# Optimization experiments

Hardware: AMD Instinct MI355X
Metric: run time of the kernel (lower is better)

The kernel has to match this reference:

```python
import jax, jax.numpy as jnp
import numpy as np

NL = 8  # number of wavenet cells


def _causal_dil_conv(x, w, b, dil):
    # x: (B, Cin, T), w: (Cout, Cin, K) -> (B, Cout, T), left-padded (causal)
    pad = (w.shape[-1] - 1) * dil
    y = jax.lax.conv_general_dilated(
        x, w, window_strides=(1,), padding=[(pad, 0)],
        rhs_dilation=(dil,), dimension_numbers=('NCH', 'OIH', 'NCH'))
    return y + b[None, :, None]


def setup_inputs() -> dict:
    key = jax.random.key(0)
    ks = jax.random.split(key, 12)
    T, B, d_lag, d_cov, d, K = 2048, 16, 1, 7, 256, 2
    s = 0.05
    return {
        'x_lag': jax.random.normal(ks[0], (T, B, d_lag), jnp.float32),
        'x_cov': jax.random.normal(ks[1], (T, B, d_cov), jnp.float32),
        'up_W': jax.random.normal(ks[2], (d_lag + d_cov, d), jnp.float32) * s,
        'up_b': jax.random.normal(ks[3], (d,), jnp.float32) * s,
        'dil_w': jax.random.normal(ks[4], (NL, 2 * d, d, K), jnp.float32) * s,
        'dil_b': jax.random.normal(ks[5], (NL, 2 * d), jnp.float32) * s,
        'skip_w': jax.random.normal(ks[6], (NL, 2 * d, d, 1), jnp.float32) * s,
        'skip_b': jax.random.normal(ks[7], (NL, 2 * d), jnp.float32) * s,
        'loc_W': jax.random.normal(ks[8], (d, 1), jnp.float32) * s,
        'loc_b': jax.random.normal(ks[9], (1,), jnp.float32) * s,
        'proj_W': jax.random.normal(ks[10], (1, 1), jnp.float32) * s,
        'proj_b': jax.random.normal(ks[11], (1,), jnp.float32) * s,
        'd_outputseqlen': 96,
    }


def reference(x_lag, x_cov, up_W, up_b, dil_w, dil_b, skip_w, skip_b,
              loc_W, loc_b, proj_W, proj_b, d_outputseqlen):
    T = x_lag.shape[0]
    h = jnp.concatenate([x_lag, x_cov[:T]], axis=-1)          # (T,B,d_lag+d_cov)
    h = h @ up_W + up_b                                        # (T,B,d)
    h = jnp.transpose(h, (1, 2, 0))                            # (B,d,T)
    skip = jnp.zeros_like(h)
    for i in range(NL):
        z = _causal_dil_conv(h, dil_w[i], dil_b[i], 2 ** i)    # (B,2d,T)
        f, g = jnp.split(z, 2, axis=1)
        gated = jnp.tanh(f) * jax.nn.sigmoid(g)                # (B,d,T)
        z2 = _causal_dil_conv(gated, skip_w[i], skip_b[i], 1)  # (B,2d,T)
        h_next, skip_next = jnp.split(z2, 2, axis=1)
        h = h + h_next
        skip = skip + skip_next
    out = jnp.transpose(skip[:, :, -d_outputseqlen:], (2, 0, 1))  # (L,B,d)
    loc = out @ loc_W + loc_b                                     # (L,B,1)
    y = jnp.transpose(loc, (1, 0, 2))[..., None]                  # (B,L,1,1)
    return y @ proj_W + proj_b                                    # (B,L,1,c_out)
```

## Files before the change

kernel.cpp:

```cpp
#include <hip/hip_runtime.h>
#include <math.h>
#include <stdint.h>

#define T_TOTAL 2048
#define NB 16
#define D 256
#define T0 1696
#define TBUF 352
#define TSKIP 1952
#define LOUT 96

typedef __bf16 bf16x8 __attribute__((ext_vector_type(8)));
typedef __bf16 bf16x4v __attribute__((ext_vector_type(4)));
typedef float f32x4 __attribute__((ext_vector_type(4)));

__device__ __forceinline__ void gload_lds16(const void* src, void* lds_dst) {
    auto g = (const __attribute__((address_space(1))) void*)(uintptr_t)src;
    auto l = (__attribute__((address_space(3))) void*)(uintptr_t)(
                 (uint32_t)(uintptr_t)lds_dst);
    __builtin_amdgcn_global_load_lds(g, l, 16, 0, 0);
}

__device__ __forceinline__ void decode_tile(int id, int ngate, int& rt, int& ct) {
    int k = id & 7;
    int j = id >> 3;
    int rpx = ngate >> 6;
    rt = k * rpx + (j >> 3);
    ct = j & 7;
}

__global__ __launch_bounds__(256) void prep_up(
    const float* __restrict__ dil_w, const float* __restrict__ skip_w,
    const float* __restrict__ x_lag, const float* __restrict__ x_cov,
    const float* __restrict__ up_W, const float* __restrict__ up_b,
    const float* __restrict__ loc_W,
    __bf16* __restrict__ wT, __bf16* __restrict__ w2, __bf16* __restrict__ w2T,
    float* __restrict__ hf, __bf16* __restrict__ hb,
    float* __restrict__ vWp)
{
    const int g0 = blockIdx.x * 256 + threadIdx.x;
    const int NT = 2048 * 256;

    for (int u = g0; u < 8 * 512 * 32; u += NT) {
        int j = u & 31;
        int cog = u >> 5;
        const float* src = dil_w + ((size_t)cog << 9) + (j << 4);
        float4 a = *(const float4*)(src);
        float4 b = *(const float4*)(src + 4);
        float4 c = *(const float4*)(src + 8);
        float4 d = *(const float4*)(src + 12);
        bf16x8 t0 = {(__bf16)a.x, (__bf16)a.z, (__bf16)b.x, (__bf16)b.z,
                     (__bf16)c.x, (__bf16)c.z, (__bf16)d.x, (__bf16)d.z};
        bf16x8 t1 = {(__bf16)a.y, (__bf16)a.w, (__bf16)b.y, (__bf16)b.w,
                     (__bf16)c.y, (__bf16)c.w, (__bf16)d.y, (__bf16)d.w};
        *(bf16x8*)(wT + ((size_t)cog << 9) + (j << 3)) = t0;
        *(bf16x8*)(wT + ((size_t)cog << 9) + 256 + (j << 3)) = t1;
    }
    for (int u = g0; u < 5 * 256 * 32; u += NT) {
        int row = u >> 5, j = u & 31;
        int ly = row >> 8, co = row & 255;
        const float* src = skip_w + (((size_t)(ly << 9) + co) << 8) + (j << 3);
        float4 a = *(const float4*)(src);
        float4 b = *(const float4*)(src + 4);
        bf16x8 v = {(__bf16)a.x, (__bf16)a.y, (__bf16)a.z, (__bf16)a.w,
                    (__bf16)b.x, (__bf16)b.y, (__bf16)b.z, (__bf16)b.w};
        *(bf16x8*)(w2 + ((size_t)row << 8) + (j << 3)) = v;
    }
    for (int u = g0; u < 2 * 256 * 32; u += NT) {
        int row = u >> 5, j = u & 31;
        int lyr = row >> 8, co = row & 255;
        int ly = 5 + lyr;
        const float* src = skip_w + (((size_t)(ly << 9) + co) << 8) + (j << 3);
        float4 a = *(const float4*)(src);
        float4 b = *(const float4*)(src + 4);
        float v[8] = {a.x, a.y, a.z, a.w, b.x, b.y, b.z, b.w};
        __bf16* wt = w2T + ((size_t)lyr << 16) + ((size_t)(j << 3) << 8) + co;
        #pragma unroll
        for (int e = 0; e < 8; ++e) wt[(size_t)e << 8] = (__bf16)v[e];
    }
    for (int u = g0; u < TBUF * NB * D; u += NT) {
        int row = u >> 8, c = u & 255;
        int tt = row >> 4, b = row & 15, t = T0 + tt;
        float acc = up_b[c] + x_lag[t * NB + b] * up_W[c];
        const float* cov = &x_cov[(t * NB + b) * 7];
        #pragma unroll
        for (int j = 0; j < 7; ++j)
            acc += cov[j] * up_W[(j + 1) * D + c];
        hf[u] = acc;
        hb[u] = (__bf16)acc;
    }
    for (int u = g0; u < 16384; u += NT) {
        int part = u >> 11;
        int r = u & 2047;
        int ly = r >> 8, ci = r & 255;
        const float* sw = skip_w + (((size_t)(ly << 9) + 256 + (part << 5)) << 8) + ci;
        float acc = 0.f;
        #pragma unroll 8
        for (int c = 0; c < 32; ++c)
            acc += sw[(size_t)c << 8] * loc_W[(part << 5) + c];
        vWp[u] = acc;
    }
}

__global__ __launch_bounds__(512, 4) void d0_kernel(
    const __bf16* __restrict__ hb, __bf16* __restrict__ gated,
    const __bf16* __restrict__ wT, const float* __restrict__ dil_b,
    const __bf16* __restrict__ w2T, const float* __restrict__ skip_b,
    __bf16* __restrict__ V, float* __restrict__ cbias,
    __bf16* __restrict__ gsv, int ngate, int tb, int M)
{
    __shared__ __align__(16) unsigned char lds[32768];
    const int id = blockIdx.x;
    const int tid = threadIdx.x;
    const int lane = tid & 63, wid = tid >> 6;
    const int wm = wid >> 1, wn = wid & 1;
    const int l15 = lane & 15, l4 = lane >> 4;
    const int ach = lane & 7;

    if (id < ngate) {
        int rt, ct;
        decode_tile(id, ngate, rt, ct);
        const int m0 = rt << 6;
        if (m0 >= M) return;
        const int cb = ct << 5;
        const int arow = (wid << 3) + (lane >> 3);
        const int aswz = (ach ^ (arow & 7)) << 3;
        const int bwid = wid & 3, bhalf = wid >> 2;
        const int brow = (bwid << 3) + (lane >> 3);
        const int bswz = (ach ^ (brow & 7)) << 3;
        const int roff1 = (tb - T0) * 16;
        const int roff0 = roff1 - 16;

        f32x4 accf = {}, accg = {};
        auto stage = [&](int t, int buf) {
            const int k0 = t << 6;
            const int ci0 = k0 & 255;
            const int roff = (t < 4) ? roff0 : roff1;
            unsigned char* base = lds + buf * 16384;
            int m = m0 + arow; if (m >= M) m = M - 1;
            gload_lds16(hb + (size_t)(m + roff) * 256 + ci0 + aswz,
                        base + (wid << 10));
            gload_lds16(wT + (size_t)(cb + bhalf * 256 + brow) * 512 + k0 + bswz,
                        base + 8192 + (bhalf << 12) + (bwid << 10));
        };
        stage(0, 0);
        for (int t = 0; t < 8; ++t) {
            const int buf = t & 1;
            if (t < 7) {
                stage(t + 1, buf ^ 1);
                asm volatile("s_waitcnt vmcnt(2)" ::: "memory");
            } else {
                asm volatile("s_waitcnt vmcnt(0)" ::: "memory");
            }
            __builtin_amdgcn_s_barrier();
            const unsigned char* base = lds + buf * 16384;
            __builtin_amdgcn_s_setprio(1);
            #pragma unroll
            for (int ks = 0; ks < 2; ++ks) {
                const int kb = (ks << 6) + (l4 << 4);
                int r = (wm << 4) + l15;
                bf16x8 av = *(const bf16x8*)(base + r * 128 + (kb ^ ((r & 7) << 4)));
                int n = (wn << 4) + l15;
                int o = n * 128 + (kb ^ ((n & 7) << 4));
                bf16x8 bfv = *(const bf16x8*)(base + 8192 + o);
                bf16x8 bgv = *(const bf16x8*)(base + 12288 + o);
                accf = __builtin_amdgcn_mfma_f32_16x16x32_bf16(av, bfv, accf, 0, 0, 0);
                accg = __builtin_amdgcn_mfma_f32_16x16x32_bf16(av, bgv, accg, 0, 0, 0);
            }
            __builtin_amdgcn_s_setprio(0);
            __builtin_amdgcn_s_barrier();
        }
        {
            const int ms0 = (TSKIP - tb) * 16;
            const int soff = (tb - TSKIP) * 16;
            int c = cb + (wn << 4) + l15;
            float bfb = dil_b[c], bgb = dil_b[c + 256];
            #pragma unroll
            for (int r = 0; r < 4; ++r) {
                int m = m0 + (wm << 4) + (l4 << 2) + r;
                if (m < M) {
                    float fv = accf[r] + bfb;
                    float gv = accg[r] + bgb;
                    float th = 2.0f / (1.0f + __expf(-2.0f * fv)) - 1.0f;
                    float sg = 1.0f / (1.0f + __expf(-gv));
                    __bf16 val = (__bf16)(th * sg);
                    gated[(size_t)m * 256 + c] = val;
                    if (m >= ms0)
                        gsv[(size_t)(m + soff) * 256 + c] = val;
                }
            }
        }
    } else if (id < ngate + 384) {
        int v = id - ngate;
        int pair = v >> 7;
        int r = v & 127;
        int tgt = (pair == 0) ? 6 : 7;
        int srcix = (pair == 2) ? 1 : 0;
        int a = r >> 6;
        int rt = (r & 63) >> 3, ct = r & 7;
        const int n0t = rt << 6;
        const int cb = ct << 5;
        const __bf16* Awt = wT + ((size_t)tgt << 18) + (a << 8);
        const __bf16* Bw = w2T + ((size_t)srcix << 16);
        const int arow = (wid << 3) + (lane >> 3);
        const int aswz = (ach ^ (arow & 7)) << 3;
        const int brow = (wid << 3) + (lane >> 3);
        const int bswz = (ach ^ (brow & 7)) << 3;

        f32x4 acc = {};
        auto stage = [&](int t, int buf) {
            const int k0 = t << 6;
            unsigned char* base = lds + buf * 12288;
            gload_lds16(Awt + (size_t)(n0t + arow) * 512 + k0 + aswz,
                        base + (wid << 10));
            if (wid < 4)
                gload_lds16(Bw + (size_t)(cb + brow) * 256 + k0 + bswz,
                            base + 8192 + (wid << 10));
        };
        stage(0, 0);
        for (int t = 0; t < 4; ++t) {
            const int buf = t & 1;
            if (t < 3) {
                stage(t + 1, buf ^ 1);
                if (wid < 4) { asm volatile("s_waitcnt vmcnt(2)" ::: "memory"); }
                else         { asm volatile("s_waitcnt vmcnt(1)" ::: "memory"); }
            } else {
                asm volatile("s_waitcnt vmcnt(0)" ::: "memory");
            }
            __builtin_amdgcn_s_barrier();
            const unsigned char* base = lds + buf * 12288;
            #pragma unroll
            for (int ks = 0; ks < 2; ++ks) {
                const int kb = (ks << 6) + (l4 << 4);
                int rr = (wm << 4) + l15;
                bf16x8 av = *(const bf16x8*)(base + rr * 128 + (kb ^ ((rr & 7) << 4)));
                int nn = (wn << 4) + l15;
                int o = nn * 128 + (kb ^ ((nn & 7) << 4));
                bf16x8 bv = *(const bf16x8*)(base + 8192 + o);
                acc = __builtin_amdgcn_mfma_f32_16x16x32_bf16(av, bv, acc, 0, 0, 0);
            }
            __builtin_amdgcn_s_barrier();
        }
        {
            int c = cb + (wn << 4) + l15;
            #pragma unroll
            for (int rr = 0; rr < 4; ++rr) {
                int n = n0t + (wm << 4) + (l4 << 2) + rr;
                V[((size_t)pair << 18) + (size_t)n * 512 + (a << 8) + c] = (__bf16)acc[rr];
            }
        }
    } else {
        int cblk = id - ngate - 384;
        int n = cblk * 8 + wid;
        int tl = n >> 9, n0 = n & 511;
        const __bf16* wrow = wT + ((size_t)(6 + tl) << 18) + ((size_t)n0 << 9);
        float s = 0.f;
        #pragma unroll
        for (int e = 0; e < 8; ++e) {
            int k = (lane << 3) + e;
            float sbv = skip_b[(5 << 9) + (k & 255)];
            if (tl == 1) sbv += skip_b[(6 << 9) + (k & 255)];
            s += sbv * (float)wrow[k];
        }
        #pragma unroll
        for (int off = 32; off; off >>= 1) s += __shfl_down(s, off);
        if (lane == 0)
            cbias[(tl << 9) + n0] = dil_b[((6 + tl) << 9) + n0] + s;
    }
}

__global__ __launch_bounds__(512, 4) void gate_n32(
    const __bf16* __restrict__ hb, __bf16* __restrict__ gout,
    const __bf16* __restrict__ wTl, const float* __restrict__ gbias,
    __bf16* __restrict__ gsv, int do_save,
    int tb, int dil, int M)
{
    __shared__ __align__(16) unsigned char lds[32768];
    int rt, ct;
    decode_tile(blockIdx.x, gridDim.x, rt, ct);
    const int m0 = rt << 6;
    if (m0 >= M) return;
    const int cb = ct << 5;
    const int tid = threadIdx.x;
    const int lane = tid & 63, wid = tid >> 6;
    const int wm = wid >> 1, wn = wid & 1;
    const int l15 = lane & 15, l4 = lane >> 4;
    const int arow = (wid << 3) + (lane >> 3);
    const int ach = lane & 7;
    const int aswz = (ach ^ (arow & 7)) << 3;
    const int bwid = wid & 3, bhalf = wid >> 2;
    const int brow = (bwid << 3) + (lane >> 3);
    const int bswz = (ach ^ (brow & 7)) << 3;
    const int roff1 = (tb - T0) * 16;
    const int roff0 = roff1 - dil * 16;

    f32x4 accf = {}, accg = {};
    auto stage = [&](int t, int buf) {
        const int k0 = t << 6;
        const int ci0 = k0 & 255;
        const int roff = (t < 4) ? roff0 : roff1;
        unsigned char* base = lds + buf * 16384;
        int m = m0 + arow; if (m >= M) m = M - 1;
        gload_lds16(hb + (size_t)(m + roff) * 256 + ci0 + aswz,
                    base + (wid << 10));
        gload_lds16(wTl + (size_t)(cb + bhalf * 256 + brow) * 512 + k0 + bswz,
                    base + 8192 + (bhalf << 12) + (bwid << 10));
    };
    stage(0, 0);
    for (int t = 0; t < 8; ++t) {
        const int buf = t & 1;
        if (t < 7) {
            stage(t + 1, buf ^ 1);
            asm volatile("s_waitcnt vmcnt(2)" ::: "memory");
        } else {
            asm volatile("s_waitcnt vmcnt(0)" ::: "memory");
        }
        __builtin_amdgcn_s_barrier();
        const unsigned char* base = lds + buf * 16384;
        __builtin_amdgcn_s_setprio(1);
        #pragma unroll
        for (int ks = 0; ks < 2; ++ks) {
            const int kb = (ks << 6) + (l4 << 4);
            int r = (wm << 4) + l15;
            bf16x8 av = *(const bf16x8*)(base + r * 128 + (kb ^ ((r & 7) << 4)));
            int n = (wn << 4) + l15;
            int o = n * 128 + (kb ^ ((n & 7) << 4));
            bf16x8 bfv = *(const bf16x8*)(base + 8192 + o);
            bf16x8 bgv = *(const bf16x8*)(base + 12288 + o);
            accf = __builtin_amdgcn_mfma_f32_16x16x32_bf16(av, bfv, accf, 0, 0, 0);
            accg = __builtin_amdgcn_mfma_f32_16x16x32_bf16(av, bgv, accg, 0, 0, 0);
        }
        __builtin_amdgcn_s_setprio(0);
        __builtin_amdgcn_s_barrier();
    }
    {
        const int ms0 = (TSKIP - tb) * 16;
        const int soff = (tb - TSKIP) * 16;
        int c = cb + (wn << 4) + l15;
        float bfb = gbias[c], bgb = gbias[c + 256];
        #pragma unroll
        for (int r = 0; r < 4; ++r) {
            int m = m0 + (wm << 4) + (l4 << 2) + r;
            if (m < M) {
                float fv = accf[r] + bfb;
                float gv = accg[r] + bgb;
                float th = 2.0f / (1.0f + __expf(-2.0f * fv)) - 1.0f;
                float sg = 1.0f / (1.0f + __expf(-gv));
                __bf16 val = (__bf16)(th * sg);
                gout[(size_t)m * 256 + c] = val;
                if (do_save && m >= ms0)
                    gsv[(size_t)(m + soff) * 256 + c] = val;
            }
        }
    }
}

__global__ __launch_bounds__(512, 4) void gate_sub(
    const __bf16* __restrict__ hb,
    const __bf16* __restrict__ g1, const __bf16* __restrict__ g2,
    __bf16* __restrict__ gout,
    const __bf16* __restrict__ Bh, const __bf16* __restrict__ Bv1,
    const __bf16* __restrict__ Bv2, const float* __restrict__ cbias_l,
    int tb, int dil, int M, int nsteps,
    int hro0, int hro1, int g1o0, int g1o1, int g2o0, int g2o1)
{
    __shared__ __align__(16) unsigned char lds[32768];
    int rt, ct;
    decode_tile(blockIdx.x, gridDim.x, rt, ct);
    const int m0 = rt << 6;
    if (m0 >= M) return;
    const int cb = ct << 5;
    const int tid = threadIdx.x;
    const int lane = tid & 63, wid = tid >> 6;
    const int wm = wid >> 1, wn = wid & 1;
    const int l15 = lane & 15, l4 = lane >> 4;
    const int arow = (wid << 3) + (lane >> 3);
    const int ach = lane & 7;
    const int aswz = (ach ^ (arow & 7)) << 3;
    const int bwid = wid & 3, bhalf = wid >> 2;
    const int brow = (bwid << 3) + (lane >> 3);
    const int bswz = (ach ^ (brow & 7)) << 3;

    f32x4 accf = {}, accg = {};
    auto stage = [&](int t, int buf) {
        unsigned char* base = lds + buf * 16384;
        int m = m0 + arow; if (m >= M) m = M - 1;
        const __bf16* asrc;
        const __bf16* bsrc;
        int ks;
        if (t < 8) {
            ks = t << 6;
            asrc = hb + (size_t)(m + ((t < 4) ? hro0 : hro1)) * 256 + (ks & 255);
            bsrc = Bh;
        } else if (t < 16) {
            ks = (t - 8) << 6;
            asrc = g1 + (size_t)(m + ((t < 12) ? g1o0 : g1o1)) * 256 + (ks & 255);
            bsrc = Bv1;
        } else {
            ks = (t - 16) << 6;
            asrc = g2 + (size_t)(m + ((t < 20) ? g2o0 : g2o1)) * 256 + (ks & 255);
            bsrc = Bv2;
        }
        gload_lds16(asrc + aswz, base + (wid << 10));
        gload_lds16(bsrc + (size_t)(cb + bhalf * 256 + brow) * 512 + ks + bswz,
                    base + 8192 + (bhalf << 12) + (bwid << 10));
    };
    stage(0, 0);
    for (int t = 0; t < nsteps; ++t) {
        const int buf = t & 1;
        if (t < nsteps - 1) {
            stage(t + 1, buf ^ 1);
            asm volatile("s_waitcnt vmcnt(2)" ::: "memory");
        } else {
            asm volatile("s_waitcnt vmcnt(0)" ::: "memory");
        }
        __builtin_amdgcn_s_barrier();
        const unsigned char* base = lds + buf * 16384;
        __builtin_amdgcn_s_setprio(1);
        #pragma unroll
        for (int ks = 0; ks < 2; ++ks) {
            const int kb = (ks << 6) + (l4 << 4);
            int r = (wm << 4) + l15;
            bf16x8 av = *(const bf16x8*)(base + r * 128 + (kb ^ ((r & 7) << 4)));
            int n = (wn << 4) + l15;
            int o = n * 128 + (kb ^ ((n & 7) << 4));
            bf16x8 bfv = *(const bf16x8*)(base + 8192 + o);
            bf16x8 bgv = *(const bf16x8*)(base + 12288 + o);
            accf = __builtin_amdgcn_mfma_f32_16x16x32_bf16(av, bfv, accf, 0, 0, 0);
            accg = __builtin_amdgcn_mfma_f32_16x16x32_bf16(av, bgv, accg, 0, 0, 0);
        }
        __builtin_amdgcn_s_setprio(0);
        __builtin_amdgcn_s_barrier();
    }
    {
        int c = cb + (wn << 4) + l15;
        float bfb = cbias_l[c], bgb = cbias_l[c + 256];
        #pragma unroll
        for (int r = 0; r < 4; ++r) {
            int m = m0 + (wm << 4) + (l4 << 2) + r;
            if (m < M) {
                float fv = accf[r] + bfb;
                float gv = accg[r] + bgb;
                float th = 2.0f / (1.0f + __expf(-2.0f * fv)) - 1.0f;
                float sg = 1.0f / (1.0f + __expf(-gv));
                gout[(size_t)m * 256 + c] = (__bf16)(th * sg);
            }
        }
    }
}

__global__ __launch_bounds__(512, 4) void skip_h(
    const __bf16* __restrict__ gated, const __bf16* __restrict__ w2l,
    float* __restrict__ hf, __bf16* __restrict__ hb,
    const float* __restrict__ sbias, int tb, int M)
{
    __shared__ __align__(16) unsigned char lds[24576];
    int rt, ct;
    decode_tile(blockIdx.x, gridDim.x, rt, ct);
    const int m0 = rt << 6;
    if (m0 >= M) return;
    const int cb = ct << 5;
    const int tid = threadIdx.x;
    const int lane = tid & 63, wid = tid >> 6;
    const int wm = wid >> 1, wn = wid & 1;
    const int l15 = lane & 15, l4 = lane >> 4;
    const int arow = (wid << 3) + (lane >> 3);
    const int ach = lane & 7;
    const int aswz = (ach ^ (arow & 7)) << 3;
    const int brow = (wid << 3) + (lane >> 3);
    const int bswz = (ach ^ (brow & 7)) << 3;
    const int roff1 = (tb - T0) * 16;

    f32x4 acch = {};
    auto stage = [&](int t, int buf) {
        const int k0 = t << 6;
        unsigned char* base = lds + buf * 12288;
        int m = m0 + arow; if (m >= M) m = M - 1;
        gload_lds16(gated + (size_t)m * 256 + k0 + aswz,
                    base + (wid << 10));
        if (wid < 4)
            gload_lds16(w2l + (size_t)(cb + brow) * 256 + k0 + bswz,
                        base + 8192 + (wid << 10));
    };
    stage(0, 0);
    for (int t = 0; t < 4; ++t) {
        const int buf = t & 1;
        if (t < 3) {
            stage(t + 1, buf ^ 1);
            if (wid < 4) { asm volatile("s_waitcnt vmcnt(2)" ::: "memory"); }
            else         { asm volatile("s_waitcnt vmcnt(1)" ::: "memory"); }
        } else {
            asm volatile("s_waitcnt vmcnt(0)" ::: "memory");
        }
        __builtin_amdgcn_s_barrier();
        const unsigned char* base = lds + buf * 12288;
        __builtin_amdgcn_s_setprio(1);
        #pragma unroll
        for (int ks = 0; ks < 2; ++ks) {
            const int kb = (ks << 6) + (l4 << 4);
            int r = (wm << 4) + l15;
            bf16x8 av = *(const bf16x8*)(base + r * 128 + (kb ^ ((r & 7) << 4)));
            int n = (wn << 4) + l15;
            int o = n * 128 + (kb ^ ((n & 7) << 4));
            bf16x8 bhv = *(const bf16x8*)(base + 8192 + o);
            acch = __builtin_amdgcn_mfma_f32_16x16x32_bf16(av, bhv, acch, 0, 0, 0);
        }
        __builtin_amdgcn_s_setprio(0);
        __builtin_amdgcn_s_barrier();
    }
    {
        int c = cb + (wn << 4) + l15;
        float bhb = sbias[c];
        #pragma unroll
        for (int r = 0; r < 4; ++r) {
            int m = m0 + (wm << 4) + (l4 << 2) + r;
            if (m < M) {
                size_t hi = (size_t)(m + roff1) * 256 + c;
                float hv = hf[hi] + acch[r] + bhb;
                hf[hi] = hv;
                hb[hi] = (__bf16)hv;
            }
        }
    }
}

__global__ __launch_bounds__(256) void final_v4(
    const __bf16* __restrict__ gsave, const __bf16* __restrict__ gA,
    const __bf16* __restrict__ gB, const __bf16* __restrict__ g7,
    const float* __restrict__ vWp, const float* __restrict__ skip_b,
    const float* __restrict__ loc_W, const float* __restrict__ loc_b,
    const float* __restrict__ proj_W, const float* __restrict__ proj_b,
    float* __restrict__ out)
{
    int tid = threadIdx.x;
    int wid = tid >> 6, lane = tid & 63;
    int o = blockIdx.x * 4 + wid;
    const __bf16* bases[8] = {
        gsave,                gsave + 1536 * 256,     gsave + 2 * 1536 * 256,
        gsave + 3 * 1536 * 256, gsave + 4 * 1536 * 256,
        gA + 3072 * 256,      gB + 2048 * 256,        g7 };
    float acc = 0.f;
    #pragma unroll
    for (int ly = 0; ly < 8; ++ly) {
        bf16x4v gv = *(const bf16x4v*)(bases[ly] + ((size_t)o << 8) + (lane << 2));
        float4 vw = {0.f, 0.f, 0.f, 0.f};
        #pragma unroll
        for (int p = 0; p < 8; ++p) {
            float4 vp = *(const float4*)(vWp + (p << 11) + (ly << 8) + (lane << 2));
            vw.x += vp.x; vw.y += vp.y; vw.z += vp.z; vw.w += vp.w;
        }
        acc += (float)gv[0] * vw.x + (float)gv[1] * vw.y
             + (float)gv[2] * vw.z + (float)gv[3] * vw.w;
    }
    #pragma unroll
    for (int j = 0; j < 32; ++j) {
        int idx = lane + (j << 6);
        int ly = idx >> 8, c = idx & 255;
        acc += skip_b[(ly << 9) + 256 + c] * loc_W[c];
    }
    #pragma unroll
    for (int off = 32; off; off >>= 1) acc += __shfl_down(acc, off);
    if (lane == 0) {
        int l = o >> 4, b = o & 15;
        out[b * LOUT + l] = (acc + loc_b[0]) * proj_W[0] + proj_b[0];
    }
}

extern "C" void kernel_launch(void* const* d_in, const int* in_sizes, int n_in,
                              void* d_out, int out_size, void* d_ws, size_t ws_size,
                              hipStream_t stream)
{
    const float* x_lag  = (const float*)d_in[0];
    const float* x_cov  = (const float*)d_in[1];
    const float* up_W   = (const float*)d_in[2];
    const float* up_b   = (const float*)d_in[3];
    const float* dil_w  = (const float*)d_in[4];
    const float* dil_b  = (const float*)d_in[5];
    const float* skip_w = (const float*)d_in[6];
    const float* skip_b = (const float*)d_in[7];
    const float* loc_W  = (const float*)d_in[8];
    const float* loc_b  = (const float*)d_in[9];
    const float* proj_W = (const float*)d_in[10];
    const float* proj_b = (const float*)d_in[11];
    float* out = (float*)d_out;

    unsigned char* ws = (unsigned char*)d_ws;
    float*  hf    = (float*)ws;
    __bf16* hb    = (__bf16*)(ws + 5767168);
    __bf16* gated = (__bf16*)(ws + 8650752);
    __bf16* gA    = (__bf16*)(ws + 11534336);
    __bf16* gB    = (__bf16*)(ws + 13893632);
    __bf16* gsave = (__bf16*)(ws + 15728640);
    __bf16* wT    = (__bf16*)(ws + 19660800);
    __bf16* w2    = (__bf16*)(ws + 23855104);
    __bf16* w2T   = (__bf16*)(ws + 24510464);
    __bf16* V     = (__bf16*)(ws + 24772608);
    float*  vWp   = (float*)(ws + 26345472);
    float*  cbias = (float*)(ws + 26411008);

    hipLaunchKernelGGL(prep_up, dim3(2048), dim3(256), 0, stream,
                       dil_w, skip_w, x_lag, x_cov, up_W, up_b, loc_W,
                       wT, w2, w2T, hf, hb, vWp);

    {
        int tb = T0 + 2, M = (T_TOTAL - tb) * NB;
        int mtp = (((M + 63) >> 6) + 7) & ~7;
        int ng0 = mtp * 8;
        hipLaunchKernelGGL(d0_kernel, dim3(ng0 + 384 + 128), dim3(512), 0, stream,
                           hb, gated, wT, dil_b, w2T, skip_b, V, cbias,
                           gsave, ng0, tb, M);
        hipLaunchKernelGGL(skip_h, dim3(ng0), dim3(512), 0, stream,
                           gated, w2, hf, hb, skip_b, tb, M);
    }
    for (int i = 1; i < 5; ++i) {
        int dil = 1 << i;
        int tb = T0 + 2 * dil;
        int M = (T_TOTAL - tb) * NB;
        int mtp = (((M + 63) >> 6) + 7) & ~7;
        hipLaunchKernelGGL(gate_n32, dim3(mtp * 8), dim3(512), 0, stream,
                           hb, gated, wT + ((size_t)i << 18),
                           dil_b + (i << 9),
                           gsave + (size_t)i * 1536 * 256, 1, tb, dil, M);
        hipLaunchKernelGGL(skip_h, dim3(mtp * 8), dim3(512), 0, stream,
                           gated, w2 + ((size_t)i << 16), hf, hb,
                           skip_b + (i << 9), tb, M);
    }
    {
        int tb = T0 + 64, M = (T_TOTAL - tb) * NB;
        int mtp = (((M + 63) >> 6) + 7) & ~7;
        hipLaunchKernelGGL(gate_n32, dim3(mtp * 8), dim3(512), 0, stream,
                           hb, gA, wT + ((size_t)5 << 18), dil_b + (5 << 9),
                           gsave, 0, tb, 32, M);
    }
    {
        int tb = T0 + 128, M = (T_TOTAL - tb) * NB;
        int mtp = (((M + 63) >> 6) + 7) & ~7;
        hipLaunchKernelGGL(gate_sub, dim3(mtp * 8), dim3(512), 0, stream,
                           hb, gA, gA, gB,
                           wT + ((size_t)6 << 18), V, V, cbias,
                           tb, 64, M, 16,
                           1024, 2048, 0, 1024, 0, 0);
    }
    {
        int tb = T0 + 256, M = (T_TOTAL - tb) * NB;
        int mtp = (((M + 63) >> 6) + 7) & ~7;
        hipLaunchKernelGGL(gate_sub, dim3(mtp * 8), dim3(512), 0, stream,
                           hb, gA, gB, gated,
                           wT + ((size_t)7 << 18), V + (1 << 18), V + (2 << 18),
                           cbias + 512,
                           tb, 128, M, 24,
                           2048, 4096, 1024, 3072, 0, 2048);
    }
    hipLaunchKernelGGL(final_v4, dim3(LOUT * NB / 4), dim3(256), 0, stream,
                       gsave, gA, gB, gated, vWp, skip_b,
                       loc_W, loc_b, proj_W, proj_b, out);
}
```

Measured before the change: 124.9 us.

## Drop fp32 residual copy and run layer 5 normally, substituting only layer 6

Removes the fp32 residual buffer hf, so the residual stream accumulates directly in bf16 and one read/write stream per skip_h goes away. Layer 5 now runs through the ordinary gate_n32/skip_h path. Only layer 6's skip output is folded algebraically into layer 7's weights (a single V matrix and one cbias), which shrinks the extra precompute in d0_kernel and simplifies the final reduction. The cost is two more launches for layer 5, a larger M for layer 6, and more rounding error because the residual sum is kept in bf16.

```diff
diff --git a/kernel.cpp b/kernel.cpp
--- a/kernel.cpp
+++ b/kernel.cpp
@@ -35,8 +35,7 @@
     const float* __restrict__ up_W, const float* __restrict__ up_b,
     const float* __restrict__ loc_W,
     __bf16* __restrict__ wT, __bf16* __restrict__ w2, __bf16* __restrict__ w2T,
-    float* __restrict__ hf, __bf16* __restrict__ hb,
-    float* __restrict__ vWp)
+    __bf16* __restrict__ hb, float* __restrict__ vWp)
 {
     const int g0 = blockIdx.x * 256 + threadIdx.x;
     const int NT = 2048 * 256;
@@ -56,7 +55,7 @@
         *(bf16x8*)(wT + ((size_t)cog << 9) + (j << 3)) = t0;
         *(bf16x8*)(wT + ((size_t)cog << 9) + 256 + (j << 3)) = t1;
     }
-    for (int u = g0; u < 5 * 256 * 32; u += NT) {
+    for (int u = g0; u < 6 * 256 * 32; u += NT) {
         int row = u >> 5, j = u & 31;
         int ly = row >> 8, co = row & 255;
         const float* src = skip_w + (((size_t)(ly << 9) + co) << 8) + (j << 3);
@@ -66,15 +65,13 @@
                     (__bf16)b.x, (__bf16)b.y, (__bf16)b.z, (__bf16)b.w};
         *(bf16x8*)(w2 + ((size_t)row << 8) + (j << 3)) = v;
     }
-    for (int u = g0; u < 2 * 256 * 32; u += NT) {
-        int row = u >> 5, j = u & 31;
-        int lyr = row >> 8, co = row & 255;
-        int ly = 5 + lyr;
-        const float* src = skip_w + (((size_t)(ly << 9) + co) << 8) + (j << 3);
+    for (int u = g0; u < 256 * 32; u += NT) {
+        int co = u >> 5, j = u & 31;
+        const float* src = skip_w + (((size_t)(6 << 9) + co) << 8) + (j << 3);
         float4 a = *(const float4*)(src);
         float4 b = *(const float4*)(src + 4);
         float v[8] = {a.x, a.y, a.z, a.w, b.x, b.y, b.z, b.w};
-        __bf16* wt = w2T + ((size_t)lyr << 16) + ((size_t)(j << 3) << 8) + co;
+        __bf16* wt = w2T + ((size_t)(j << 3) << 8) + co;
         #pragma unroll
         for (int e = 0; e < 8; ++e) wt[(size_t)e << 8] = (__bf16)v[e];
     }
@@ -86,7 +83,6 @@
         #pragma unroll
         for (int j = 0; j < 7; ++j)
             acc += cov[j] * up_W[(j + 1) * D + c];
-        hf[u] = acc;
         hb[u] = (__bf16)acc;
     }
     for (int u = g0; u < 16384; u += NT) {
@@ -190,18 +186,14 @@
                 }
             }
         }
-    } else if (id < ngate + 384) {
+    } else if (id < ngate + 128) {
         int v = id - ngate;
-        int pair = v >> 7;
-        int r = v & 127;
-        int tgt = (pair == 0) ? 6 : 7;
-        int srcix = (pair == 2) ? 1 : 0;
-        int a = r >> 6;
-        int rt = (r & 63) >> 3, ct = r & 7;
+        int a = v >> 6;
+        int r = v & 63;
+        int rt = r >> 3, ct = r & 7;
         const int n0t = rt << 6;
         const int cb = ct << 5;
-        const __bf16* Awt = wT + ((size_t)tgt << 18) + (a << 8);
-        const __bf16* Bw = w2T + ((size_t)srcix << 16);
+        const __bf16* Awt = wT + ((size_t)7 << 18) + (a << 8);
         const int arow = (wid << 3) + (lane >> 3);
         const int aswz = (ach ^ (arow & 7)) << 3;
         const int brow = (wid << 3) + (lane >> 3);
@@ -214,7 +206,7 @@
             gload_lds16(Awt + (size_t)(n0t + arow) * 512 + k0 + aswz,
                         base + (wid << 10));
             if (wid < 4)
-                gload_lds16(Bw + (size_t)(cb + brow) * 256 + k0 + bswz,
+                gload_lds16(w2T + (size_t)(cb + brow) * 256 + k0 + bswz,
                             base + 8192 + (wid << 10));
         };
         stage(0, 0);
@@ -246,26 +238,23 @@
             #pragma unroll
             for (int rr = 0; rr < 4; ++rr) {
                 int n = n0t + (wm << 4) + (l4 << 2) + rr;
-                V[((size_t)pair << 18) + (size_t)n * 512 + (a << 8) + c] = (__bf16)acc[rr];
+                V[(size_t)n * 512 + (a << 8) + c] = (__bf16)acc[rr];
             }
         }
     } else {
-        int cblk = id - ngate - 384;
+        int cblk = id - ngate - 128;
         int n = cblk * 8 + wid;
-        int tl = n >> 9, n0 = n & 511;
-        const __bf16* wrow = wT + ((size_t)(6 + tl) << 18) + ((size_t)n0 << 9);
+        const __bf16* wrow = wT + ((size_t)7 << 18) + ((size_t)n << 9);
         float s = 0.f;
         #pragma unroll
         for (int e = 0; e < 8; ++e) {
             int k = (lane << 3) + e;
-            float sbv = skip_b[(5 << 9) + (k & 255)];
-            if (tl == 1) sbv += skip_b[(6 << 9) + (k & 255)];
-            s += sbv * (float)wrow[k];
+            s += skip_b[(6 << 9) + (k & 255)] * (float)wrow[k];
         }
         #pragma unroll
         for (int off = 32; off; off >>= 1) s += __shfl_down(s, off);
         if (lane == 0)
-            cbias[(tl << 9) + n0] = dil_b[((6 + tl) << 9) + n0] + s;
+            cbias[n] = dil_b[(7 << 9) + n] + s;
     }
 }
 
@@ -355,14 +344,11 @@
     }
 }
 
-__global__ __launch_bounds__(512, 4) void gate_sub(
-    const __bf16* __restrict__ hb,
-    const __bf16* __restrict__ g1, const __bf16* __restrict__ g2,
-    __bf16* __restrict__ gout,
-    const __bf16* __restrict__ Bh, const __bf16* __restrict__ Bv1,
-    const __bf16* __restrict__ Bv2, const float* __restrict__ cbias_l,
-    int tb, int dil, int M, int nsteps,
-    int hro0, int hro1, int g1o0, int g1o1, int g2o0, int g2o1)
+__global__ __launch_bounds__(512, 4) void gate7_sub(
+    const __bf16* __restrict__ hb, const __bf16* __restrict__ g6,
+    __bf16* __restrict__ g7,
+    const __bf16* __restrict__ wT7, const __bf16* __restrict__ Vl,
+    const float* __restrict__ cb7, int M)
 {
     __shared__ __align__(16) unsigned char lds[32768];
     int rt, ct;
@@ -385,30 +371,27 @@
     auto stage = [&](int t, int buf) {
         unsigned char* base = lds + buf * 16384;
         int m = m0 + arow; if (m >= M) m = M - 1;
-        const __bf16* asrc;
-        const __bf16* bsrc;
-        int ks;
         if (t < 8) {
-            ks = t << 6;
-            asrc = hb + (size_t)(m + ((t < 4) ? hro0 : hro1)) * 256 + (ks & 255);
-            bsrc = Bh;
-        } else if (t < 16) {
-            ks = (t - 8) << 6;
-            asrc = g1 + (size_t)(m + ((t < 12) ? g1o0 : g1o1)) * 256 + (ks & 255);
-            bsrc = Bv1;
+            const int k0 = t << 6;
+            const int roff = (t < 4) ? 2048 : 4096;
+            gload_lds16(hb + (size_t)(m + roff) * 256 + (k0 & 255) + aswz,
+                        base + (wid << 10));
+            gload_lds16(wT7 + (size_t)(cb + bhalf * 256 + brow) * 512 + k0 + bswz,
+                        base + 8192 + (bhalf << 12) + (bwid << 10));
         } else {
-            ks = (t - 16) << 6;
-            asrc = g2 + (size_t)(m + ((t < 20) ? g2o0 : g2o1)) * 256 + (ks & 255);
-            bsrc = Bv2;
-        }
-        gload_lds16(asrc + aswz, base + (wid << 10));
-        gload_lds16(bsrc + (size_t)(cb + bhalf * 256 + brow) * 512 + ks + bswz,
-                    base + 8192 + (bhalf << 12) + (bwid << 10));
+            const int k0 = (t - 8) << 6;
+            const int goff = (t < 12) ? 0 : 2048;
+            gload_lds16(g6 + (size_t)(m + goff) * 256 + (k0 & 255) + aswz,
+                        base + (wid << 10));
+            gload_lds16(Vl + (size_t)(cb + bhalf * 256 + brow) * 512 + k0 + bswz,
+                        base + 8192 + (bhalf << 12) + (bwid << 10));
+        }
     };
     stage(0, 0);
-    for (int t = 0; t < nsteps; ++t) {
+    #pragma unroll
+    for (int t = 0; t < 16; ++t) {
         const int buf = t & 1;
-        if (t < nsteps - 1) {
+        if (t < 15) {
             stage(t + 1, buf ^ 1);
             asm volatile("s_waitcnt vmcnt(2)" ::: "memory");
         } else {
@@ -434,7 +417,7 @@
     }
     {
         int c = cb + (wn << 4) + l15;
-        float bfb = cbias_l[c], bgb = cbias_l[c + 256];
+        float bfb = cb7[c], bgb = cb7[c + 256];
         #pragma unroll
         for (int r = 0; r < 4; ++r) {
             int m = m0 + (wm << 4) + (l4 << 2) + r;
@@ -443,7 +426,7 @@
                 float gv = accg[r] + bgb;
                 float th = 2.0f / (1.0f + __expf(-2.0f * fv)) - 1.0f;
                 float sg = 1.0f / (1.0f + __expf(-gv));
-                gout[(size_t)m * 256 + c] = (__bf16)(th * sg);
+                g7[(size_t)m * 256 + c] = (__bf16)(th * sg);
             }
         }
     }
@@ -451,8 +434,7 @@
 
 __global__ __launch_bounds__(512, 4) void skip_h(
     const __bf16* __restrict__ gated, const __bf16* __restrict__ w2l,
-    float* __restrict__ hf, __bf16* __restrict__ hb,
-    const float* __restrict__ sbias, int tb, int M)
+    __bf16* __restrict__ hb, const float* __restrict__ sbias, int tb, int M)
 {
     __shared__ __align__(16) unsigned char lds[24576];
     int rt, ct;
@@ -516,17 +498,16 @@
             int m = m0 + (wm << 4) + (l4 << 2) + r;
             if (m < M) {
                 size_t hi = (size_t)(m + roff1) * 256 + c;
-                float hv = hf[hi] + acch[r] + bhb;
-                hf[hi] = hv;
+                float hv = (float)hb[hi] + acch[r] + bhb;
                 hb[hi] = (__bf16)hv;
             }
         }
     }
 }
 
-__global__ __launch_bounds__(256) void final_v4(
-    const __bf16* __restrict__ gsave, const __bf16* __restrict__ gA,
-    const __bf16* __restrict__ gB, const __bf16* __restrict__ g7,
+__global__ __launch_bounds__(256) void final_v5(
+    const __bf16* __restrict__ gsave, const __bf16* __restrict__ gated,
+    const __bf16* __restrict__ g7,
     const float* __restrict__ vWp, const float* __restrict__ skip_b,
     const float* __restrict__ loc_W, const float* __restrict__ loc_b,
     const float* __restrict__ proj_W, const float* __restrict__ proj_b,
@@ -536,9 +517,9 @@
     int wid = tid >> 6, lane = tid & 63;
     int o = blockIdx.x * 4 + wid;
     const __bf16* bases[8] = {
-        gsave,                gsave + 1536 * 256,     gsave + 2 * 1536 * 256,
-        gsave + 3 * 1536 * 256, gsave + 4 * 1536 * 256,
-        gA + 3072 * 256,      gB + 2048 * 256,        g7 };
+        gsave,                  gsave + 1536 * 256,     gsave + 2 * 1536 * 256,
+        gsave + 3 * 1536 * 256, gsave + 4 * 1536 * 256, gsave + 5 * 1536 * 256,
+        gated + 2048 * 256,     g7 };
     float acc = 0.f;
     #pragma unroll
     for (int ly = 0; ly < 8; ++ly) {
@@ -585,34 +566,32 @@
     float* out = (float*)d_out;
 
     unsigned char* ws = (unsigned char*)d_ws;
-    float*  hf    = (float*)ws;
-    __bf16* hb    = (__bf16*)(ws + 5767168);
-    __bf16* gated = (__bf16*)(ws + 8650752);
-    __bf16* gA    = (__bf16*)(ws + 11534336);
-    __bf16* gB    = (__bf16*)(ws + 13893632);
-    __bf16* gsave = (__bf16*)(ws + 15728640);
-    __bf16* wT    = (__bf16*)(ws + 19660800);
-    __bf16* w2    = (__bf16*)(ws + 23855104);
-    __bf16* w2T   = (__bf16*)(ws + 24510464);
-    __bf16* V     = (__bf16*)(ws + 24772608);
-    float*  vWp   = (float*)(ws + 26345472);
-    float*  cbias = (float*)(ws + 26411008);
+    __bf16* hb    = (__bf16*)ws;
+    __bf16* gated = (__bf16*)(ws + 2883584);
+    __bf16* g7    = (__bf16*)(ws + 5767168);
+    __bf16* gsave = (__bf16*)(ws + 6553600);
+    __bf16* wT    = (__bf16*)(ws + 11272192);
+    __bf16* w2    = (__bf16*)(ws + 15466496);
+    __bf16* w2T   = (__bf16*)(ws + 16252928);
+    __bf16* V     = (__bf16*)(ws + 16384000);
+    float*  vWp   = (float*)(ws + 16908288);
+    float*  cbias = (float*)(ws + 16973824);
 
     hipLaunchKernelGGL(prep_up, dim3(2048), dim3(256), 0, stream,
                        dil_w, skip_w, x_lag, x_cov, up_W, up_b, loc_W,
-                       wT, w2, w2T, hf, hb, vWp);
+                       wT, w2, w2T, hb, vWp);
 
     {
         int tb = T0 + 2, M = (T_TOTAL - tb) * NB;
         int mtp = (((M + 63) >> 6) + 7) & ~7;
         int ng0 = mtp * 8;
-        hipLaunchKernelGGL(d0_kernel, dim3(ng0 + 384 + 128), dim3(512), 0, stream,
+        hipLaunchKernelGGL(d0_kernel, dim3(ng0 + 128 + 64), dim3(512), 0, stream,
                            hb, gated, wT, dil_b, w2T, skip_b, V, cbias,
                            gsave, ng0, tb, M);
         hipLaunchKernelGGL(skip_h, dim3(ng0), dim3(512), 0, stream,
-                           gated, w2, hf, hb, skip_b, tb, M);
-    }
-    for (int i = 1; i < 5; ++i) {
+                           gated, w2, hb, skip_b, tb, M);
+    }
+    for (int i = 1; i < 6; ++i) {
         int dil = 1 << i;
         int tb = T0 + 2 * dil;
         int M = (T_TOTAL - tb) * NB;
@@ -622,36 +601,23 @@
                            dil_b + (i << 9),
                            gsave + (size_t)i * 1536 * 256, 1, tb, dil, M);
         hipLaunchKernelGGL(skip_h, dim3(mtp * 8), dim3(512), 0, stream,
-                           gated, w2 + ((size_t)i << 16), hf, hb,
+                           gated, w2 + ((size_t)i << 16), hb,
                            skip_b + (i << 9), tb, M);
-    }
-    {
-        int tb = T0 + 64, M = (T_TOTAL - tb) * NB;
-        int mtp = (((M + 63) >> 6) + 7) & ~7;
-        hipLaunchKernelGGL(gate_n32, dim3(mtp * 8), dim3(512), 0, stream,
-                           hb, gA, wT + ((size_t)5 << 18), dil_b + (5 << 9),
-                           gsave, 0, tb, 32, M);
     }
     {
         int tb = T0 + 128, M = (T_TOTAL - tb) * NB;
         int mtp = (((M + 63) >> 6) + 7) & ~7;
-        hipLaunchKernelGGL(gate_sub, dim3(mtp * 8), dim3(512), 0, stream,
-                           hb, gA, gA, gB,
-                           wT + ((size_t)6 << 18), V, V, cbias,
-                           tb, 64, M, 16,
-                           1024, 2048, 0, 1024, 0, 0);
+        hipLaunchKernelGGL(gate_n32, dim3(mtp * 8), dim3(512), 0, stream,
+                           hb, gated, wT + ((size_t)6 << 18), dil_b + (6 << 9),
+                           gsave, 0, tb, 64, M);
     }
     {
-        int tb = T0 + 256, M = (T_TOTAL - tb) * NB;
+        int M = 1536;
         int mtp = (((M + 63) >> 6) + 7) & ~7;
-        hipLaunchKernelGGL(gate_sub, dim3(mtp * 8), dim3(512), 0, stream,
-                           hb, gA, gB, gated,
-                           wT + ((size_t)7 << 18), V + (1 << 18), V + (2 << 18),
-                           cbias + 512,
-                           tb, 128, M, 24,
-                           2048, 4096, 1024, 3072, 0, 2048);
-    }
-    hipLaunchKernelGGL(final_v4, dim3(LOUT * NB / 4), dim3(256), 0, stream,
-                       gsave, gA, gB, gated, vWp, skip_b,
+        hipLaunchKernelGGL(gate7_sub, dim3(mtp * 8), dim3(512), 0, stream,
+                           hb, gated, g7, wT + ((size_t)7 << 18), V, cbias, M);
+    }
+    hipLaunchKernelGGL(final_v5, dim3(LOUT * NB / 4), dim3(256), 0, stream,
+                       gsave, gated, g7, vWp, skip_b,
                        loc_W, loc_b, proj_W, proj_b, out);
 }
```

Result: faster. 110.1 us (-11.9%).

## Drop fp32 residual buffer, keep h in bf16 only; templatize gate_sub

Applied to the files above, without the earlier changes.

Removes the fp32 copy of the residual stream h. skip_h now reads the residual from the bf16 buffer, adds the update in fp32 and writes bf16 back, which cuts the per-layer read-modify-write traffic on the residual. gate_sub is made a template with compile-time step counts and offsets, and its loop is fully unrolled. Layer 7's gate output moves to a separate g7 buffer and the workspace is repacked. The cost is that bf16 rounding now accumulates in the residual across the eight layers, which lowers accuracy.

```diff
diff --git a/kernel.cpp b/kernel.cpp
--- a/kernel.cpp
+++ b/kernel.cpp
@@ -35,8 +35,7 @@
     const float* __restrict__ up_W, const float* __restrict__ up_b,
     const float* __restrict__ loc_W,
     __bf16* __restrict__ wT, __bf16* __restrict__ w2, __bf16* __restrict__ w2T,
-    float* __restrict__ hf, __bf16* __restrict__ hb,
-    float* __restrict__ vWp)
+    __bf16* __restrict__ hb, float* __restrict__ vWp)
 {
     const int g0 = blockIdx.x * 256 + threadIdx.x;
     const int NT = 2048 * 256;
@@ -86,7 +85,6 @@
         #pragma unroll
         for (int j = 0; j < 7; ++j)
             acc += cov[j] * up_W[(j + 1) * D + c];
-        hf[u] = acc;
         hb[u] = (__bf16)acc;
     }
     for (int u = g0; u < 16384; u += NT) {
@@ -355,14 +353,13 @@
     }
 }
 
+template<int NSTEPS, int HRO0, int HRO1, int G1O0, int G1O1, int G2O0, int G2O1>
 __global__ __launch_bounds__(512, 4) void gate_sub(
     const __bf16* __restrict__ hb,
     const __bf16* __restrict__ g1, const __bf16* __restrict__ g2,
     __bf16* __restrict__ gout,
     const __bf16* __restrict__ Bh, const __bf16* __restrict__ Bv1,
-    const __bf16* __restrict__ Bv2, const float* __restrict__ cbias_l,
-    int tb, int dil, int M, int nsteps,
-    int hro0, int hro1, int g1o0, int g1o1, int g2o0, int g2o1)
+    const __bf16* __restrict__ Bv2, const float* __restrict__ cbias_l, int M)
 {
     __shared__ __align__(16) unsigned char lds[32768];
     int rt, ct;
@@ -390,15 +387,15 @@
         int ks;
         if (t < 8) {
             ks = t << 6;
-            asrc = hb + (size_t)(m + ((t < 4) ? hro0 : hro1)) * 256 + (ks & 255);
+            asrc = hb + (size_t)(m + ((t < 4) ? HRO0 : HRO1)) * 256 + (ks & 255);
             bsrc = Bh;
         } else if (t < 16) {
             ks = (t - 8) << 6;
-            asrc = g1 + (size_t)(m + ((t < 12) ? g1o0 : g1o1)) * 256 + (ks & 255);
+            asrc = g1 + (size_t)(m + ((t < 12) ? G1O0 : G1O1)) * 256 + (ks & 255);
             bsrc = Bv1;
         } else {
             ks = (t - 16) << 6;
-            asrc = g2 + (size_t)(m + ((t < 20) ? g2o0 : g2o1)) * 256 + (ks & 255);
+            asrc = g2 + (size_t)(m + ((t < 20) ? G2O0 : G2O1)) * 256 + (ks & 255);
             bsrc = Bv2;
         }
         gload_lds16(asrc + aswz, base + (wid << 10));
@@ -406,9 +403,10 @@
                     base + 8192 + (bhalf << 12) + (bwid << 10));
     };
     stage(0, 0);
-    for (int t = 0; t < nsteps; ++t) {
+    #pragma unroll
+    for (int t = 0; t < NSTEPS; ++t) {
         const int buf = t & 1;
-        if (t < nsteps - 1) {
+        if (t < NSTEPS - 1) {
             stage(t + 1, buf ^ 1);
             asm volatile("s_waitcnt vmcnt(2)" ::: "memory");
         } else {
@@ -451,8 +449,7 @@
 
 __global__ __launch_bounds__(512, 4) void skip_h(
     const __bf16* __restrict__ gated, const __bf16* __restrict__ w2l,
-    float* __restrict__ hf, __bf16* __restrict__ hb,
-    const float* __restrict__ sbias, int tb, int M)
+    __bf16* __restrict__ hb, const float* __restrict__ sbias, int tb, int M)
 {
     __shared__ __align__(16) unsigned char lds[24576];
     int rt, ct;
@@ -516,15 +513,14 @@
             int m = m0 + (wm << 4) + (l4 << 2) + r;
             if (m < M) {
                 size_t hi = (size_t)(m + roff1) * 256 + c;
-                float hv = hf[hi] + acch[r] + bhb;
-                hf[hi] = hv;
+                float hv = (float)hb[hi] + acch[r] + bhb;
                 hb[hi] = (__bf16)hv;
             }
         }
     }
 }
 
-__global__ __launch_bounds__(256) void final_v4(
+__global__ __launch_bounds__(256) void final_v6(
     const __bf16* __restrict__ gsave, const __bf16* __restrict__ gA,
     const __bf16* __restrict__ gB, const __bf16* __restrict__ g7,
     const float* __restrict__ vWp, const float* __restrict__ skip_b,
@@ -536,9 +532,9 @@
     int wid = tid >> 6, lane = tid & 63;
     int o = blockIdx.x * 4 + wid;
     const __bf16* bases[8] = {
-        gsave,                gsave + 1536 * 256,     gsave + 2 * 1536 * 256,
+        gsave,                  gsave + 1536 * 256,     gsave + 2 * 1536 * 256,
         gsave + 3 * 1536 * 256, gsave + 4 * 1536 * 256,
-        gA + 3072 * 256,      gB + 2048 * 256,        g7 };
+        gA + 3072 * 256,        gB + 2048 * 256,        g7 };
     float acc = 0.f;
     #pragma unroll
     for (int ly = 0; ly < 8; ++ly) {
@@ -585,22 +581,22 @@
     float* out = (float*)d_out;
 
     unsigned char* ws = (unsigned char*)d_ws;
-    float*  hf    = (float*)ws;
-    __bf16* hb    = (__bf16*)(ws + 5767168);
-    __bf16* gated = (__bf16*)(ws + 8650752);
-    __bf16* gA    = (__bf16*)(ws + 11534336);
-    __bf16* gB    = (__bf16*)(ws + 13893632);
-    __bf16* gsave = (__bf16*)(ws + 15728640);
-    __bf16* wT    = (__bf16*)(ws + 19660800);
-    __bf16* w2    = (__bf16*)(ws + 23855104);
-    __bf16* w2T   = (__bf16*)(ws + 24510464);
-    __bf16* V     = (__bf16*)(ws + 24772608);
-    float*  vWp   = (float*)(ws + 26345472);
-    float*  cbias = (float*)(ws + 26411008);
+    __bf16* hb    = (__bf16*)ws;
+    __bf16* gated = (__bf16*)(ws + 2883584);
+    __bf16* gA    = (__bf16*)(ws + 5767168);
+    __bf16* gB    = (__bf16*)(ws + 8126464);
+    __bf16* g7    = (__bf16*)(ws + 9961472);
+    __bf16* gsave = (__bf16*)(ws + 10747904);
+    __bf16* wT    = (__bf16*)(ws + 14680064);
+    __bf16* w2    = (__bf16*)(ws + 18874368);
+    __bf16* w2T   = (__bf16*)(ws + 19529728);
+    __bf16* V     = (__bf16*)(ws + 19791872);
+    float*  vWp   = (float*)(ws + 21364736);
+    float*  cbias = (float*)(ws + 21430272);
 
     hipLaunchKernelGGL(prep_up, dim3(2048), dim3(256), 0, stream,
                        dil_w, skip_w, x_lag, x_cov, up_W, up_b, loc_W,
-                       wT, w2, w2T, hf, hb, vWp);
+                       wT, w2, w2T, hb, vWp);
 
     {
         int tb = T0 + 2, M = (T_TOTAL - tb) * NB;
@@ -610,7 +606,7 @@
                            hb, gated, wT, dil_b, w2T, skip_b, V, cbias,
                            gsave, ng0, tb, M);
         hipLaunchKernelGGL(skip_h, dim3(ng0), dim3(512), 0, stream,
-                           gated, w2, hf, hb, skip_b, tb, M);
+                           gated, w2, hb, skip_b, tb, M);
     }
     for (int i = 1; i < 5; ++i) {
         int dil = 1 << i;
@@ -622,7 +618,7 @@
                            dil_b + (i << 9),
                            gsave + (size_t)i * 1536 * 256, 1, tb, dil, M);
         hipLaunchKernelGGL(skip_h, dim3(mtp * 8), dim3(512), 0, stream,
-                           gated, w2 + ((size_t)i << 16), hf, hb,
+                           gated, w2 + ((size_t)i << 16), hb,
                            skip_b + (i << 9), tb, M);
     }
     {
@@ -633,25 +629,23 @@
                            gsave, 0, tb, 32, M);
     }
     {
-        int tb = T0 + 128, M = (T_TOTAL - tb) * NB;
+        int M = 3584;
         int mtp = (((M + 63) >> 6) + 7) & ~7;
-        hipLaunchKernelGGL(gate_sub, dim3(mtp * 8), dim3(512), 0, stream,
+        hipLaunchKernelGGL((gate_sub<16, 1024, 2048, 0, 1024, 0, 0>),
+                           dim3(mtp * 8), dim3(512), 0, stream,
                            hb, gA, gA, gB,
-                           wT + ((size_t)6 << 18), V, V, cbias,
-                           tb, 64, M, 16,
-                           1024, 2048, 0, 1024, 0, 0);
+                           wT + ((size_t)6 << 18), V, V, cbias, M);
     }
     {
-        int tb = T0 + 256, M = (T_TOTAL - tb) * NB;
+        int M = 1536;
         int mtp = (((M + 63) >> 6) + 7) & ~7;
-        hipLaunchKernelGGL(gate_sub, dim3(mtp * 8), dim3(512), 0, stream,
-                           hb, gA, gB, gated,
+        hipLaunchKernelGGL((gate_sub<24, 2048, 4096, 1024, 3072, 0, 2048>),
+                           dim3(mtp * 8), dim3(512), 0, stream,
+                           hb, gA, gB, g7,
                            wT + ((size_t)7 << 18), V + (1 << 18), V + (2 << 18),
-                           cbias + 512,
-                           tb, 128, M, 24,
-                           2048, 4096, 1024, 3072, 0, 2048);
-    }
-    hipLaunchKernelGGL(final_v4, dim3(LOUT * NB / 4), dim3(256), 0, stream,
-                       gsave, gA, gB, gated, vWp, skip_b,
+                           cbias + 512, M);
+    }
+    hipLaunchKernelGGL(final_v6, dim3(LOUT * NB / 4), dim3(256), 0, stream,
+                       gsave, gA, gB, g7, vWp, skip_b,
                        loc_W, loc_b, proj_W, proj_b, out);
 }
```

Result: faster. 114.8 us (-8.1%).
